# Kernel tuning notes

Measured on AMD Instinct MI355X. Metric: run time of the kernel, lower is better.

## Reference

```python
import jax, jax.numpy as jnp
import numpy as np
from jax import lax

K = 3
STRIDE = 1
PAD = 1
DIL = 1
EPS = 1e-5


def conv2d(x, w, b):
    y = lax.conv_general_dilated(
        x, w, (STRIDE, STRIDE), [(PAD, PAD), (PAD, PAD)],
        rhs_dilation=(DIL, DIL), dimension_numbers=('NCHW', 'OIHW', 'NCHW'))
    return y + b[None, :, None, None]


def deform_conv(x, offset, w):
    # x: [B,C,H,W], offset: [B,2*K2,Ho,Wo] (dy,dx interleaved per tap), w: [O,C,K,K]
    B, C, H, W = x.shape
    O = w.shape[0]
    K2 = K * K
    Ho, Wo = offset.shape[2], offset.shape[3]
    ky, kx = jnp.meshgrid(jnp.arange(K), jnp.arange(K), indexing='ij')
    # base sampling grid per kernel tap: [K2,Ho,Wo] (broadcast)
    by = (ky.reshape(K2, 1, 1) * DIL).astype(x.dtype) + (jnp.arange(Ho) * STRIDE - PAD).astype(x.dtype).reshape(1, Ho, 1)
    bx = (kx.reshape(K2, 1, 1) * DIL).astype(x.dtype) + (jnp.arange(Wo) * STRIDE - PAD).astype(x.dtype).reshape(1, 1, Wo)
    off = offset.reshape(B, K2, 2, Ho, Wo)
    py = by[None] + off[:, :, 0]  # [B,K2,Ho,Wo]
    px = bx[None] + off[:, :, 1]
    y0 = jnp.floor(py)
    x0 = jnp.floor(px)
    wy = py - y0
    wx = px - x0
    y0i = y0.astype(jnp.int32)
    x0i = x0.astype(jnp.int32)
    x_flat = x.reshape(B, C, H * W)

    def corner(yi, xi, cw):
        valid = ((yi >= 0) & (yi < H) & (xi >= 0) & (xi < W)).astype(x.dtype)
        idx = (jnp.clip(yi, 0, H - 1) * W + jnp.clip(xi, 0, W - 1)).reshape(B, -1)
        v = jax.vmap(lambda xb, ib: xb[:, ib])(x_flat, idx)  # [B,C,K2*Ho*Wo]
        return v * (cw * valid).reshape(B, 1, -1)

    val = (corner(y0i, x0i, (1 - wy) * (1 - wx))
           + corner(y0i, x0i + 1, (1 - wy) * wx)
           + corner(y0i + 1, x0i, wy * (1 - wx))
           + corner(y0i + 1, x0i + 1, wy * wx))  # [B,C,K2*Ho*Wo]
    samp = val.reshape(B, C, K2, Ho * Wo)
    out = jnp.einsum('bckp,ock->bop', samp, w.reshape(O, C, K2))
    return out.reshape(B, O, Ho, Wo)


def bn_gelu(x, gamma, beta):
    m = x.mean((0, 2, 3), keepdims=True)
    v = x.var((0, 2, 3), keepdims=True)
    xn = (x - m) / jnp.sqrt(v + EPS) * gamma[None, :, None, None] + beta[None, :, None, None]
    return jax.nn.gelu(xn, approximate=False)


def deform_block(x, w_off, b_off, w_def, gamma, beta):
    offset = conv2d(x, w_off, b_off)
    return bn_gelu(deform_conv(x, offset, w_def), gamma, beta)


def setup_inputs() -> dict:
    key = jax.random.key(0)
    ks = jax.random.split(key, 8)
    B, C, H, W = 4, 128, 112, 112
    fan = C * K * K
    x = jax.random.normal(ks[0], (B, C, H, W), jnp.float32)
    # offset conv weights: small random (original inits to 0; randomized to exercise sampling)
    w_off1 = jax.random.normal(ks[1], (2 * K * K, C, K, K), jnp.float32) * 0.01
    b_off1 = jnp.zeros((2 * K * K,), jnp.float32)
    w_def1 = jax.random.normal(ks[2], (C, C, K, K), jnp.float32) / np.sqrt(fan)
    gamma1 = jnp.ones((C,), jnp.float32)
    beta1 = jnp.zeros((C,), jnp.float32)
    w_off2 = jax.random.normal(ks[3], (2 * K * K, C, K, K), jnp.float32) * 0.01
    b_off2 = jnp.zeros((2 * K * K,), jnp.float32)
    w_def2 = jax.random.normal(ks[4], (C, C, K, K), jnp.float32) / np.sqrt(fan)
    gamma2 = jnp.ones((C,), jnp.float32)
    beta2 = jnp.zeros((C,), jnp.float32)
    return dict(x=x, w_off1=w_off1, b_off1=b_off1, w_def1=w_def1, gamma1=gamma1, beta1=beta1,
                w_off2=w_off2, b_off2=b_off2, w_def2=w_def2, gamma2=gamma2, beta2=beta2)


def reference(x, w_off1, b_off1, w_def1, gamma1, beta1,
              w_off2, b_off2, w_def2, gamma2, beta2):
    inp = x
    x = deform_block(x, w_off1, b_off1, w_def1, gamma1, beta1)
    x = deform_block(x, w_off2, b_off2, w_def2, gamma2, beta2)
    return x + inp
```

## Files before the change

### kernel.cpp

```cpp
#include <hip/hip_runtime.h>
#include <hip/hip_bf16.h>
#include <math.h>

#define HW 12544
#define CC 128
#define BB 4

typedef short bf16x8 __attribute__((ext_vector_type(8)));
typedef float f32x4 __attribute__((ext_vector_type(4)));

__device__ __forceinline__ float bf2f(unsigned int u) {
  union { unsigned int i; float f; } v; v.i = u << 16; return v.f;
}
__device__ __forceinline__ unsigned short f2bf(float f) {
  __hip_bfloat16 h = __float2bfloat16(f);
  return *reinterpret_cast<unsigned short*>(&h);
}
__device__ __forceinline__ float gelu(float v) {
  return 0.5f * v * (1.f + erff(v * 0.70710678118654752f));
}
__device__ __forceinline__ unsigned uc4(const uint4& v, int q) {
  return q == 0 ? v.x : q == 1 ? v.y : q == 2 ? v.z : v.w;
}

__global__ __launch_bounds__(256) void to_nhwc(const float* __restrict__ x,
                                               unsigned short* __restrict__ xh) {
  const int pt = blockIdx.x, ct = blockIdx.y, b = blockIdx.z;
  const int p0 = pt * 32, c0 = ct * 32;
  const int tid = threadIdx.x;
  __shared__ float ls[32][33];
  int col = tid & 31, r = tid >> 5;
#pragma unroll
  for (int i = 0; i < 4; i++) {
    int c = c0 + r + i * 8;
    ls[r + i * 8][col] = x[((size_t)(b * CC) + c) * HW + p0 + col];
  }
  __syncthreads();
  int px = tid >> 3, cq = (tid & 7) * 4;
  ushort4 v;
  v.x = f2bf(ls[cq + 0][px]);
  v.y = f2bf(ls[cq + 1][px]);
  v.z = f2bf(ls[cq + 2][px]);
  v.w = f2bf(ls[cq + 3][px]);
  *(ushort4*)&xh[((size_t)(b * HW) + p0 + px) * CC + c0 + cq] = v;
}

__global__ void pack_all(const float* __restrict__ wd1, const float* __restrict__ wo1,
                         const float* __restrict__ wd2, const float* __restrict__ wo2,
                         unsigned short* __restrict__ wpk1, unsigned short* __restrict__ wopk1,
                         unsigned short* __restrict__ wpk2, unsigned short* __restrict__ wopk2) {
  int i = blockIdx.x * 256 + threadIdx.x;
  if (i < 294912) {
    int ii = (i < 147456) ? i : i - 147456;
    const float* src = (i < 147456) ? wd1 : wd2;
    unsigned short* dst = (i < 147456) ? wpk1 : wpk2;
    int j = ii & 7, lane = (ii >> 3) & 63, ks = (ii >> 9) & 3, mo = (ii >> 11) & 7, k2 = ii >> 14;
    int o = mo * 16 + (lane & 15), c = ks * 32 + ((lane >> 4) << 3) + j;
    dst[ii] = f2bf(src[(o * CC + c) * 9 + k2]);
  } else {
    int ii = i - 294912;
    const float* src = (ii < 36864) ? wo1 : wo2;
    unsigned short* dst = (ii < 36864) ? wopk1 : wopk2;
    ii = (ii < 36864) ? ii : ii - 36864;
    int j = ii & 7, lane = (ii >> 3) & 63, ks = (ii >> 9) & 3, mo = (ii >> 11) & 1, k2 = ii >> 12;
    int o = mo * 16 + (lane & 15), c = ks * 32 + ((lane >> 4) << 3) + j;
    dst[ii] = (o < 18) ? f2bf(src[(o * CC + c) * 9 + k2]) : (unsigned short)0;
  }
}

__global__ __launch_bounds__(256) void offset_mfma(
    const unsigned short* __restrict__ xh, const unsigned short* __restrict__ wopk,
    const float* __restrict__ boff, float* __restrict__ offs2) {
  const int bid0 = blockIdx.x;
  const int bid = (bid0 & 7) * 196 + (bid0 >> 3);
  const int b = bid / 392;
  const int p0 = (bid % 392) * 32;
  const int tid = threadIdx.x;
  const int l = tid & 63, w = tid >> 6;
  const int hl = l & 15, ph = l >> 4;
  const int row = l & 15, grp = l >> 4;
  const int pxg = (w >> 1) * 16;
  const int mw = w & 1;
  __shared__ unsigned short s_smp[2][4096];
  const unsigned short* xb = xh + (size_t)b * HW * CC + hl * 8;
  f32x4 acc = (f32x4){0.f, 0.f, 0.f, 0.f};
  uint4 g2[2];
  bf16x8 af[4];

#define OISSUE(K2T)                                                            \
  {                                                                            \
    int ky = (K2T) / 3, kx = (K2T) % 3;                                        \
    _Pragma("unroll") for (int s = 0; s < 2; s++) {                            \
      int pxl = w * 8 + s * 4 + ph;                                            \
      int p = p0 + pxl;                                                        \
      int ho = p / 112, wo = p - ho * 112;                                     \
      int y = ho + ky - 1, x = wo + kx - 1;                                    \
      uint4 t = make_uint4(0u, 0u, 0u, 0u);                                    \
      if (((unsigned)y < 112u) & ((unsigned)x < 112u))                         \
        t = *(const uint4*)&xb[(size_t)(y * 112 + x) * CC];                    \
      g2[s] = t;                                                               \
    }                                                                          \
  }

#define OCOMMIT(BNBUF)                                                         \
  _Pragma("unroll") for (int s = 0; s < 2; s++) {                              \
    int pxl = w * 8 + s * 4 + ph;                                              \
    *(uint4*)((char*)&s_smp[BNBUF][0] +                                        \
              ((pxl * 256 + hl * 16) ^ ((pxl & 7) << 4))) = g2[s];             \
  }

#define OMFMA(BCBUF, ksB)                                                      \
  __builtin_amdgcn_s_setprio(1);                                               \
  _Pragma("unroll") for (int ks = ksB; ks < ksB + 2; ks++) {                   \
    int pxr = pxg + row;                                                       \
    bf16x8 bfr = *(const bf16x8*)((const char*)&s_smp[BCBUF][0] +              \
                 ((pxr * 256 + ks * 64 + grp * 16) ^ ((pxr & 7) << 4)));       \
    acc = __builtin_amdgcn_mfma_f32_16x16x32_bf16(af[ks], bfr, acc, 0, 0, 0);  \
  }                                                                            \
  __builtin_amdgcn_s_setprio(0);

#define OLOADW(K2T)                                                            \
  {                                                                            \
    const unsigned short* wb = wopk + (size_t)(K2T) * 4096;                    \
    _Pragma("unroll") for (int ks = 0; ks < 4; ks++)                           \
      af[ks] = *(const bf16x8*)&wb[(mw * 4 + ks) * 512 + l * 8];               \
  }

#define OITER(K2T, BC, BN)                                                     \
  {                                                                            \
    if ((K2T) < 8) { OISSUE((K2T) + 1); }                                      \
    OMFMA(BC, 0);                                                              \
    if ((K2T) < 8) { OCOMMIT(BN); }                                            \
    OMFMA(BC, 2);                                                              \
    if ((K2T) < 8) { OLOADW((K2T) + 1); __syncthreads(); }                     \
  }

  OISSUE(0); OCOMMIT(0); OLOADW(0);
  __syncthreads();
  OITER(0, 0, 1) OITER(1, 1, 0) OITER(2, 0, 1) OITER(3, 1, 0) OITER(4, 0, 1)
  OITER(5, 1, 0) OITER(6, 0, 1) OITER(7, 1, 0) OITER(8, 0, 1)
#undef OISSUE
#undef OCOMMIT
#undef OMFMA
#undef OLOADW
#undef OITER

  int p = p0 + pxg + row;
  if (mw == 0) {
    float2 w0 = make_float2(acc[0] + boff[grp * 4 + 0], acc[1] + boff[grp * 4 + 1]);
    float2 w1 = make_float2(acc[2] + boff[grp * 4 + 2], acc[3] + boff[grp * 4 + 3]);
    *(float2*)&offs2[((size_t)(b * 9 + grp * 2) * HW + p) * 2] = w0;
    *(float2*)&offs2[((size_t)(b * 9 + grp * 2 + 1) * HW + p) * 2] = w1;
  } else if (grp == 0) {
    float2 w2 = make_float2(acc[0] + boff[16], acc[1] + boff[17]);
    *(float2*)&offs2[((size_t)(b * 9 + 8) * HW + p) * 2] = w2;
  }
}

__global__ __launch_bounds__(256, 3) void deform_mfma(
    const unsigned short* __restrict__ xh, const float* __restrict__ offs2,
    const unsigned short* __restrict__ wpk, unsigned short* __restrict__ zh,
    float* __restrict__ part) {
  const int bid0 = blockIdx.x;
  const int bid = (bid0 & 7) * 196 + (bid0 >> 3);
  const int b = bid / 392;
  const int p0 = (bid % 392) * 32;
  const int tid = threadIdx.x;
  const int l = tid & 63, w = tid >> 6;
  const int hl = l & 15, ph = l >> 4;
  const int row = l & 15, grp = l >> 4;
  __shared__ unsigned short s_smp[2][4096];
  __shared__ uint4 s_coord[9][32];

  for (int e = tid; e < 288; e += 256) {
    int k2 = e >> 5, px = e & 31;
    int p = p0 + px;
    int ho = p / 112, wo = p - ho * 112;
    int ky = k2 / 3, kx = k2 - 3 * ky;
    float2 dv = *(const float2*)&offs2[((size_t)(b * 9 + k2) * HW + p) * 2];
    float py = (float)(ho + ky - 1) + dv.x;
    float pxf = (float)(wo + kx - 1) + dv.y;
    float y0f = floorf(py), x0f = floorf(pxf);
    float wy = py - y0f, wx = pxf - x0f;
    int y0 = (int)y0f, x0 = (int)x0f;
    int y1 = y0 + 1, x1 = x0 + 1;
    bool iy0 = ((unsigned)y0 < 112u), iy1 = ((unsigned)y1 < 112u);
    bool ix0 = ((unsigned)x0 < 112u), ix1 = ((unsigned)x1 < 112u);
    float v00 = (iy0 & ix0) ? (1.f - wy) * (1.f - wx) : 0.f;
    float v01 = (iy0 & ix1) ? (1.f - wy) * wx : 0.f;
    float v10 = (iy1 & ix0) ? wy * (1.f - wx) : 0.f;
    float v11 = (iy1 & ix1) ? wy * wx : 0.f;
    int y0c = min(max(y0, 0), 111), y1c = min(max(y1, 0), 111);
    int x0c = min(max(x0, 0), 111), x1c = min(max(x1, 0), 111);
    uint4 ce;
    ce.x = (unsigned)(y0c * 112 + x0c) | ((unsigned)(y0c * 112 + x1c) << 16);
    ce.y = (unsigned)(y1c * 112 + x0c) | ((unsigned)(y1c * 112 + x1c) << 16);
    ce.z = (unsigned)f2bf(v00) | ((unsigned)f2bf(v01) << 16);
    ce.w = (unsigned)f2bf(v10) | ((unsigned)f2bf(v11) << 16);
    s_coord[k2][px] = ce;
  }

  const unsigned short* xb = xh + (size_t)b * HW * CC + hl * 8;
  f32x4 acc[2][2];
#pragma unroll
  for (int m = 0; m < 2; m++)
#pragma unroll
    for (int n = 0; n < 2; n++) acc[m][n] = (f32x4){0.f, 0.f, 0.f, 0.f};
  uint4 g[2][4];
  uint2 wts[2];
  bf16x8 af[2][4];
  __syncthreads();

#define DISSUE(K2T)                                                            \
  _Pragma("unroll") for (int s = 0; s < 2; s++) {                              \
    int pxl = w * 8 + s * 4 + ph;                                              \
    uint4 cc = s_coord[K2T][pxl];                                              \
    wts[s] = make_uint2(cc.z, cc.w);                                           \
    g[s][0] = *(const uint4*)&xb[(size_t)(cc.x & 0xffffu) * CC];               \
    g[s][1] = *(const uint4*)&xb[(size_t)(cc.x >> 16) * CC];                   \
    g[s][2] = *(const uint4*)&xb[(size_t)(cc.y & 0xffffu) * CC];               \
    g[s][3] = *(const uint4*)&xb[(size_t)(cc.y >> 16) * CC];                   \
  }

#define DCOMMIT(BNBUF)                                                         \
  _Pragma("unroll") for (int s = 0; s < 2; s++) {                              \
    int pxl = w * 8 + s * 4 + ph;                                              \
    float w00 = bf2f(wts[s].x & 0xffffu), w01 = bf2f(wts[s].x >> 16);          \
    float w10 = bf2f(wts[s].y & 0xffffu), w11 = bf2f(wts[s].y >> 16);          \
    unsigned rr[4];                                                            \
    _Pragma("unroll") for (int q = 0; q < 4; q++) {                            \
      unsigned a0 = uc4(g[s][0], q), a1 = uc4(g[s][1], q);                     \
      unsigned a2 = uc4(g[s][2], q), a3 = uc4(g[s][3], q);                     \
      float elo = w00 * bf2f(a0 & 0xffffu) + w01 * bf2f(a1 & 0xffffu)          \
                + w10 * bf2f(a2 & 0xffffu) + w11 * bf2f(a3 & 0xffffu);         \
      float ehi = w00 * bf2f(a0 >> 16) + w01 * bf2f(a1 >> 16)                  \
                + w10 * bf2f(a2 >> 16) + w11 * bf2f(a3 >> 16);                 \
      rr[q] = (unsigned)f2bf(elo) | ((unsigned)f2bf(ehi) << 16);               \
    }                                                                          \
    *(uint4*)((char*)&s_smp[BNBUF][0] +                                        \
              ((pxl * 256 + hl * 16) ^ ((pxl & 7) << 4))) =                    \
        make_uint4(rr[0], rr[1], rr[2], rr[3]);                                \
  }

#define DMFMA(BCBUF, ksB)                                                      \
  __builtin_amdgcn_s_setprio(1);                                               \
  _Pragma("unroll") for (int ks = ksB; ks < ksB + 2; ks++) {                   \
    bf16x8 bfr[2];                                                             \
    _Pragma("unroll") for (int n = 0; n < 2; n++) {                            \
      int pxr = n * 16 + row;                                                  \
      bfr[n] = *(const bf16x8*)((const char*)&s_smp[BCBUF][0] +                \
               ((pxr * 256 + ks * 64 + grp * 16) ^ ((pxr & 7) << 4)));         \
    }                                                                          \
    _Pragma("unroll") for (int m = 0; m < 2; m++)                              \
      _Pragma("unroll") for (int n = 0; n < 2; n++)                            \
        acc[m][n] = __builtin_amdgcn_mfma_f32_16x16x32_bf16(af[m][ks], bfr[n], acc[m][n], 0, 0, 0); \
  }                                                                            \
  __builtin_amdgcn_s_setprio(0);

#define DLOADW(K2T)                                                            \
  {                                                                            \
    const unsigned short* wb = wpk + (size_t)((K2T) * 8 + w * 2) * 2048;       \
    _Pragma("unroll") for (int m = 0; m < 2; m++)                              \
      _Pragma("unroll") for (int ks = 0; ks < 4; ks++)                         \
        af[m][ks] = *(const bf16x8*)&wb[(m * 4 + ks) * 512 + l * 8];           \
  }

#define DITER(K2T, BC, BN)                                                     \
  {                                                                            \
    if ((K2T) < 8) { DISSUE((K2T) + 1); }                                      \
    DMFMA(BC, 0);                                                              \
    if ((K2T) < 8) { DCOMMIT(BN); }                                            \
    DMFMA(BC, 2);                                                              \
    if ((K2T) < 8) { DLOADW((K2T) + 1); __syncthreads(); }                     \
  }

  DISSUE(0); DCOMMIT(0); DLOADW(0);
  __syncthreads();
  DITER(0, 0, 1) DITER(1, 1, 0) DITER(2, 0, 1) DITER(3, 1, 0) DITER(4, 0, 1)
  DITER(5, 1, 0) DITER(6, 0, 1) DITER(7, 1, 0) DITER(8, 0, 1)
#undef DISSUE
#undef DCOMMIT
#undef DMFMA
#undef DLOADW
#undef DITER

#pragma unroll
  for (int m = 0; m < 2; m++)
#pragma unroll
    for (int n = 0; n < 2; n++) {
      int o = (w * 2 + m) * 16 + grp * 4;
      size_t px = (size_t)(b * HW) + p0 + n * 16 + row;
      unsigned lo = (unsigned)f2bf(acc[m][n][0]) | ((unsigned)f2bf(acc[m][n][1]) << 16);
      unsigned hi = (unsigned)f2bf(acc[m][n][2]) | ((unsigned)f2bf(acc[m][n][3]) << 16);
      *(uint2*)&zh[px * CC + o] = make_uint2(lo, hi);
    }

  float sv[8], qv[8];
#pragma unroll
  for (int m = 0; m < 2; m++)
#pragma unroll
    for (int r = 0; r < 4; r++) {
      float s = 0.f, q = 0.f;
#pragma unroll
      for (int n = 0; n < 2; n++) { float v = acc[m][n][r]; s += v; q += v * v; }
      sv[m * 4 + r] = s; qv[m * 4 + r] = q;
    }
#pragma unroll
  for (int d = 1; d < 16; d <<= 1)
#pragma unroll
    for (int i = 0; i < 8; i++) {
      sv[i] += __shfl_xor(sv[i], d);
      qv[i] += __shfl_xor(qv[i], d);
    }
  if (row == 0) {
#pragma unroll
    for (int m = 0; m < 2; m++)
#pragma unroll
      for (int r = 0; r < 4; r++) {
        int ch = (w * 2 + m) * 16 + grp * 4 + r;
        part[(size_t)ch * 1568 + bid] = sv[m * 4 + r];
        part[(size_t)(128 + ch) * 1568 + bid] = qv[m * 4 + r];
      }
  }
}

__global__ __launch_bounds__(256) void bn_fin(const float* __restrict__ part,
                                              const float* __restrict__ gamma,
                                              const float* __restrict__ beta,
                                              float* __restrict__ stats) {
  const int c = blockIdx.x, t = threadIdx.x;
  float s = 0.f, q = 0.f;
  for (int j = t; j < 1568; j += 256) {
    s += part[(size_t)c * 1568 + j];
    q += part[(size_t)(128 + c) * 1568 + j];
  }
  __shared__ float ss[256], sq2[256];
  ss[t] = s; sq2[t] = q;
  __syncthreads();
  for (int d = 128; d > 0; d >>= 1) {
    if (t < d) { ss[t] += ss[t + d]; sq2[t] += sq2[t + d]; }
    __syncthreads();
  }
  if (t == 0) {
    float N = 50176.f;
    float m = ss[0] / N;
    float var = sq2[0] / N - m * m;
    stats[c] = m;
    stats[128 + c] = rsqrtf(var + 1e-5f) * gamma[c];
    stats[256 + c] = beta[c];
  }
}

__global__ __launch_bounds__(256) void bn_gelu_to_bf16(
    const unsigned short* __restrict__ zh, const float* __restrict__ stats,
    unsigned short* __restrict__ yh) {
  int i = blockIdx.x * 256 + threadIdx.x;
  int c0 = (i & 15) * 8;
  uint4 zv = ((const uint4*)zh)[i];
  f32x4 m0 = *(const f32x4*)&stats[c0], m1 = *(const f32x4*)&stats[c0 + 4];
  f32x4 r0 = *(const f32x4*)&stats[128 + c0], r1 = *(const f32x4*)&stats[128 + c0 + 4];
  f32x4 b0 = *(const f32x4*)&stats[256 + c0], b1 = *(const f32x4*)&stats[256 + c0 + 4];
  float v[8] = {bf2f(zv.x & 0xffffu), bf2f(zv.x >> 16), bf2f(zv.y & 0xffffu), bf2f(zv.y >> 16),
                bf2f(zv.z & 0xffffu), bf2f(zv.z >> 16), bf2f(zv.w & 0xffffu), bf2f(zv.w >> 16)};
  unsigned o[4];
#pragma unroll
  for (int j = 0; j < 4; j++) {
    float mj0 = (j < 2) ? m0[j * 2] : m1[j * 2 - 4], mj1 = (j < 2) ? m0[j * 2 + 1] : m1[j * 2 - 3];
    float rj0 = (j < 2) ? r0[j * 2] : r1[j * 2 - 4], rj1 = (j < 2) ? r0[j * 2 + 1] : r1[j * 2 - 3];
    float bj0 = (j < 2) ? b0[j * 2] : b1[j * 2 - 4], bj1 = (j < 2) ? b0[j * 2 + 1] : b1[j * 2 - 3];
    float e0 = gelu((v[j * 2] - mj0) * rj0 + bj0);
    float e1 = gelu((v[j * 2 + 1] - mj1) * rj1 + bj1);
    o[j] = (unsigned)f2bf(e0) | ((unsigned)f2bf(e1) << 16);
  }
  ((uint4*)yh)[i] = make_uint4(o[0], o[1], o[2], o[3]);
}

__global__ __launch_bounds__(256) void bn_gelu_final(
    const unsigned short* __restrict__ zh, const float* __restrict__ stats,
    const float* __restrict__ x, float* __restrict__ out) {
  const int pt = blockIdx.x, b = blockIdx.y;
  const int p0 = pt * 16;
  const int tid = threadIdx.x;
  __shared__ float ls[16][129];
  {
    int cq = tid & 15, r = tid >> 4;
    uint4 zv = *(const uint4*)&zh[((size_t)(b * HW) + p0 + r) * CC + cq * 8];
    float v[8] = {bf2f(zv.x & 0xffffu), bf2f(zv.x >> 16), bf2f(zv.y & 0xffffu), bf2f(zv.y >> 16),
                  bf2f(zv.z & 0xffffu), bf2f(zv.z >> 16), bf2f(zv.w & 0xffffu), bf2f(zv.w >> 16)};
    f32x4 m0 = *(const f32x4*)&stats[cq * 8], m1 = *(const f32x4*)&stats[cq * 8 + 4];
    f32x4 r0 = *(const f32x4*)&stats[128 + cq * 8], r1 = *(const f32x4*)&stats[128 + cq * 8 + 4];
    f32x4 b0 = *(const f32x4*)&stats[256 + cq * 8], b1 = *(const f32x4*)&stats[256 + cq * 8 + 4];
#pragma unroll
    for (int j = 0; j < 4; j++) {
      ls[r][cq * 8 + j] = gelu((v[j] - m0[j]) * r0[j] + b0[j]);
      ls[r][cq * 8 + 4 + j] = gelu((v[4 + j] - m1[j]) * r1[j] + b1[j]);
    }
  }
  __syncthreads();
  int c = tid & 127, half = tid >> 7;
  const float* xr = x + ((size_t)(b * CC) + c) * HW + p0 + half * 8;
  float* orow = out + ((size_t)(b * CC) + c) * HW + p0 + half * 8;
  float4 o1 = make_float4(ls[half * 8 + 0][c], ls[half * 8 + 1][c],
                          ls[half * 8 + 2][c], ls[half * 8 + 3][c]);
  float4 o2 = make_float4(ls[half * 8 + 4][c], ls[half * 8 + 5][c],
                          ls[half * 8 + 6][c], ls[half * 8 + 7][c]);
  float4 x1 = *(const float4*)&xr[0];
  float4 x2 = *(const float4*)&xr[4];
  o1.x += x1.x; o1.y += x1.y; o1.z += x1.z; o1.w += x1.w;
  o2.x += x2.x; o2.y += x2.y; o2.z += x2.z; o2.w += x2.w;
  *(float4*)&orow[0] = o1;
  *(float4*)&orow[4] = o2;
}

extern "C" void kernel_launch(void* const* d_in, const int* in_sizes, int n_in,
                              void* d_out, int out_size, void* d_ws, size_t ws_size,
                              hipStream_t stream) {
  const float* x = (const float*)d_in[0];
  const float* w_off1 = (const float*)d_in[1];
  const float* b_off1 = (const float*)d_in[2];
  const float* w_def1 = (const float*)d_in[3];
  const float* gamma1 = (const float*)d_in[4];
  const float* beta1 = (const float*)d_in[5];
  const float* w_off2 = (const float*)d_in[6];
  const float* b_off2 = (const float*)d_in[7];
  const float* w_def2 = (const float*)d_in[8];
  const float* gamma2 = (const float*)d_in[9];
  const float* beta2 = (const float*)d_in[10];
  float* out = (float*)d_out;

  char* ws = (char*)d_ws;
  unsigned short* xhb = (unsigned short*)ws;
  unsigned short* zhb = (unsigned short*)(ws + 12845056);
  float* offb = (float*)(ws + 25690112);
  unsigned short* wpk1 = (unsigned short*)(ws + 29302784);
  unsigned short* wpk2 = (unsigned short*)(ws + 29597696);
  unsigned short* wopk1 = (unsigned short*)(ws + 29892608);
  unsigned short* wopk2 = (unsigned short*)(ws + 29966336);
  float* partb = (float*)(ws + 30040064);
  float* statsb = (float*)(ws + 31645696);

  to_nhwc<<<dim3(392, 4, 4), 256, 0, stream>>>(x, xhb);
  pack_all<<<1440, 256, 0, stream>>>(w_def1, w_off1, w_def2, w_off2,
                                     wpk1, wopk1, wpk2, wopk2);

  offset_mfma<<<1568, 256, 0, stream>>>(xhb, wopk1, b_off1, offb);
  deform_mfma<<<1568, 256, 0, stream>>>(xhb, offb, wpk1, zhb, partb);
  bn_fin<<<128, 256, 0, stream>>>(partb, gamma1, beta1, statsb);
  bn_gelu_to_bf16<<<3136, 256, 0, stream>>>(zhb, statsb, xhb);

  offset_mfma<<<1568, 256, 0, stream>>>(xhb, wopk2, b_off2, offb);
  deform_mfma<<<1568, 256, 0, stream>>>(xhb, offb, wpk2, zhb, partb);
  bn_fin<<<128, 256, 0, stream>>>(partb, gamma2, beta2, statsb);
  bn_gelu_final<<<dim3(784, 4), 256, 0, stream>>>(zhb, statsb, x, out);
}
```

Baseline: 172.5 us.

## Halve deform conv pixel tile to 16 per block, doubling grid size

Shrinks the per-block pixel tile in the deformable conv kernel from 32 to 16 pixels, so each wave gathers one pixel group per tap instead of two and issues half as many MFMAs per weight fragment. The grid doubles to 3136 blocks, which adds parallelism and cuts per-thread registers and LDS, which may help occupancy. In exchange, each weight fragment load is reused over fewer pixels, and the BN partial-sum buffer and its reduction double in size. The stats buffer offset moves to make room for the larger partials.

```diff
diff --git a/kernel.cpp b/kernel.cpp
--- a/kernel.cpp
+++ b/kernel.cpp
@@ -162,18 +162,18 @@
     const unsigned short* __restrict__ wpk, unsigned short* __restrict__ zh,
     float* __restrict__ part) {
   const int bid0 = blockIdx.x;
-  const int bid = (bid0 & 7) * 196 + (bid0 >> 3);
-  const int b = bid / 392;
-  const int p0 = (bid % 392) * 32;
+  const int bid = (bid0 & 7) * 392 + (bid0 >> 3);
+  const int b = bid / 784;
+  const int p0 = (bid % 784) * 16;
   const int tid = threadIdx.x;
   const int l = tid & 63, w = tid >> 6;
   const int hl = l & 15, ph = l >> 4;
   const int row = l & 15, grp = l >> 4;
-  __shared__ unsigned short s_smp[2][4096];
-  __shared__ uint4 s_coord[9][32];
-
-  for (int e = tid; e < 288; e += 256) {
-    int k2 = e >> 5, px = e & 31;
+  __shared__ unsigned short s_smp[2][2048];
+  __shared__ uint4 s_coord[9][16];
+
+  for (int e = tid; e < 144; e += 256) {
+    int k2 = e >> 4, px = e & 15;
     int p = p0 + px;
     int ho = p / 112, wo = p - ho * 112;
     int ky = k2 / 3, kx = k2 - 3 * ky;
@@ -201,36 +201,34 @@
   }
 
   const unsigned short* xb = xh + (size_t)b * HW * CC + hl * 8;
-  f32x4 acc[2][2];
-#pragma unroll
-  for (int m = 0; m < 2; m++)
-#pragma unroll
-    for (int n = 0; n < 2; n++) acc[m][n] = (f32x4){0.f, 0.f, 0.f, 0.f};
-  uint4 g[2][4];
-  uint2 wts[2];
+  f32x4 acc[2];
+  acc[0] = (f32x4){0.f, 0.f, 0.f, 0.f};
+  acc[1] = (f32x4){0.f, 0.f, 0.f, 0.f};
+  uint4 g[4];
+  uint2 wts;
   bf16x8 af[2][4];
   __syncthreads();
 
 #define DISSUE(K2T)                                                            \
-  _Pragma("unroll") for (int s = 0; s < 2; s++) {                              \
-    int pxl = w * 8 + s * 4 + ph;                                              \
+  {                                                                            \
+    int pxl = w * 4 + ph;                                                      \
     uint4 cc = s_coord[K2T][pxl];                                              \
-    wts[s] = make_uint2(cc.z, cc.w);                                           \
-    g[s][0] = *(const uint4*)&xb[(size_t)(cc.x & 0xffffu) * CC];               \
-    g[s][1] = *(const uint4*)&xb[(size_t)(cc.x >> 16) * CC];                   \
-    g[s][2] = *(const uint4*)&xb[(size_t)(cc.y & 0xffffu) * CC];               \
-    g[s][3] = *(const uint4*)&xb[(size_t)(cc.y >> 16) * CC];                   \
+    wts = make_uint2(cc.z, cc.w);                                              \
+    g[0] = *(const uint4*)&xb[(size_t)(cc.x & 0xffffu) * CC];                  \
+    g[1] = *(const uint4*)&xb[(size_t)(cc.x >> 16) * CC];                      \
+    g[2] = *(const uint4*)&xb[(size_t)(cc.y & 0xffffu) * CC];                  \
+    g[3] = *(const uint4*)&xb[(size_t)(cc.y >> 16) * CC];                      \
   }
 
 #define DCOMMIT(BNBUF)                                                         \
-  _Pragma("unroll") for (int s = 0; s < 2; s++) {                              \
-    int pxl = w * 8 + s * 4 + ph;                                              \
-    float w00 = bf2f(wts[s].x & 0xffffu), w01 = bf2f(wts[s].x >> 16);          \
-    float w10 = bf2f(wts[s].y & 0xffffu), w11 = bf2f(wts[s].y >> 16);          \
+  {                                                                            \
+    int pxl = w * 4 + ph;                                                      \
+    float w00 = bf2f(wts.x & 0xffffu), w01 = bf2f(wts.x >> 16);                \
+    float w10 = bf2f(wts.y & 0xffffu), w11 = bf2f(wts.y >> 16);                \
     unsigned rr[4];                                                            \
     _Pragma("unroll") for (int q = 0; q < 4; q++) {                            \
-      unsigned a0 = uc4(g[s][0], q), a1 = uc4(g[s][1], q);                     \
-      unsigned a2 = uc4(g[s][2], q), a3 = uc4(g[s][3], q);                     \
+      unsigned a0 = uc4(g[0], q), a1 = uc4(g[1], q);                           \
+      unsigned a2 = uc4(g[2], q), a3 = uc4(g[3], q);                           \
       float elo = w00 * bf2f(a0 & 0xffffu) + w01 * bf2f(a1 & 0xffffu)          \
                 + w10 * bf2f(a2 & 0xffffu) + w11 * bf2f(a3 & 0xffffu);         \
       float ehi = w00 * bf2f(a0 >> 16) + w01 * bf2f(a1 >> 16)                  \
@@ -245,15 +243,10 @@
 #define DMFMA(BCBUF, ksB)                                                      \
   __builtin_amdgcn_s_setprio(1);                                               \
   _Pragma("unroll") for (int ks = ksB; ks < ksB + 2; ks++) {                   \
-    bf16x8 bfr[2];                                                             \
-    _Pragma("unroll") for (int n = 0; n < 2; n++) {                            \
-      int pxr = n * 16 + row;                                                  \
-      bfr[n] = *(const bf16x8*)((const char*)&s_smp[BCBUF][0] +                \
-               ((pxr * 256 + ks * 64 + grp * 16) ^ ((pxr & 7) << 4)));         \
-    }                                                                          \
+    bf16x8 bfr = *(const bf16x8*)((const char*)&s_smp[BCBUF][0] +              \
+               ((row * 256 + ks * 64 + grp * 16) ^ ((row & 7) << 4)));         \
     _Pragma("unroll") for (int m = 0; m < 2; m++)                              \
-      _Pragma("unroll") for (int n = 0; n < 2; n++)                            \
-        acc[m][n] = __builtin_amdgcn_mfma_f32_16x16x32_bf16(af[m][ks], bfr[n], acc[m][n], 0, 0, 0); \
+      acc[m] = __builtin_amdgcn_mfma_f32_16x16x32_bf16(af[m][ks], bfr, acc[m], 0, 0, 0); \
   }                                                                            \
   __builtin_amdgcn_s_setprio(0);
 
@@ -285,25 +278,22 @@
 #undef DITER
 
 #pragma unroll
+  for (int m = 0; m < 2; m++) {
+    int o = (w * 2 + m) * 16 + grp * 4;
+    size_t px = (size_t)(b * HW) + p0 + row;
+    unsigned lo = (unsigned)f2bf(acc[m][0]) | ((unsigned)f2bf(acc[m][1]) << 16);
+    unsigned hi = (unsigned)f2bf(acc[m][2]) | ((unsigned)f2bf(acc[m][3]) << 16);
+    *(uint2*)&zh[px * CC + o] = make_uint2(lo, hi);
+  }
+
+  float sv[8], qv[8];
+#pragma unroll
   for (int m = 0; m < 2; m++)
 #pragma unroll
-    for (int n = 0; n < 2; n++) {
-      int o = (w * 2 + m) * 16 + grp * 4;
-      size_t px = (size_t)(b * HW) + p0 + n * 16 + row;
-      unsigned lo = (unsigned)f2bf(acc[m][n][0]) | ((unsigned)f2bf(acc[m][n][1]) << 16);
-      unsigned hi = (unsigned)f2bf(acc[m][n][2]) | ((unsigned)f2bf(acc[m][n][3]) << 16);
-      *(uint2*)&zh[px * CC + o] = make_uint2(lo, hi);
-    }
-
-  float sv[8], qv[8];
-#pragma unroll
-  for (int m = 0; m < 2; m++)
-#pragma unroll
     for (int r = 0; r < 4; r++) {
-      float s = 0.f, q = 0.f;
-#pragma unroll
-      for (int n = 0; n < 2; n++) { float v = acc[m][n][r]; s += v; q += v * v; }
-      sv[m * 4 + r] = s; qv[m * 4 + r] = q;
+      float v = acc[m][r];
+      sv[m * 4 + r] = v;
+      qv[m * 4 + r] = v * v;
     }
 #pragma unroll
   for (int d = 1; d < 16; d <<= 1)
@@ -318,8 +308,8 @@
 #pragma unroll
       for (int r = 0; r < 4; r++) {
         int ch = (w * 2 + m) * 16 + grp * 4 + r;
-        part[(size_t)ch * 1568 + bid] = sv[m * 4 + r];
-        part[(size_t)(128 + ch) * 1568 + bid] = qv[m * 4 + r];
+        part[(size_t)ch * 3136 + bid] = sv[m * 4 + r];
+        part[(size_t)(128 + ch) * 3136 + bid] = qv[m * 4 + r];
       }
   }
 }
@@ -330,9 +320,9 @@
                                               float* __restrict__ stats) {
   const int c = blockIdx.x, t = threadIdx.x;
   float s = 0.f, q = 0.f;
-  for (int j = t; j < 1568; j += 256) {
-    s += part[(size_t)c * 1568 + j];
-    q += part[(size_t)(128 + c) * 1568 + j];
+  for (int j = t; j < 3136; j += 256) {
+    s += part[(size_t)c * 3136 + j];
+    q += part[(size_t)(128 + c) * 3136 + j];
   }
   __shared__ float ss[256], sq2[256];
   ss[t] = s; sq2[t] = q;
@@ -437,19 +427,19 @@
   unsigned short* wopk1 = (unsigned short*)(ws + 29892608);
   unsigned short* wopk2 = (unsigned short*)(ws + 29966336);
   float* partb = (float*)(ws + 30040064);
-  float* statsb = (float*)(ws + 31645696);
+  float* statsb = (float*)(ws + 33251328);
 
   to_nhwc<<<dim3(392, 4, 4), 256, 0, stream>>>(x, xhb);
   pack_all<<<1440, 256, 0, stream>>>(w_def1, w_off1, w_def2, w_off2,
                                      wpk1, wopk1, wpk2, wopk2);
 
   offset_mfma<<<1568, 256, 0, stream>>>(xhb, wopk1, b_off1, offb);
-  deform_mfma<<<1568, 256, 0, stream>>>(xhb, offb, wpk1, zhb, partb);
+  deform_mfma<<<3136, 256, 0, stream>>>(xhb, offb, wpk1, zhb, partb);
   bn_fin<<<128, 256, 0, stream>>>(partb, gamma1, beta1, statsb);
   bn_gelu_to_bf16<<<3136, 256, 0, stream>>>(zhb, statsb, xhb);
 
   offset_mfma<<<1568, 256, 0, stream>>>(xhb, wopk2, b_off2, offb);
-  deform_mfma<<<1568, 256, 0, stream>>>(xhb, offb, wpk2, zhb, partb);
+  deform_mfma<<<3136, 256, 0, stream>>>(xhb, offb, wpk2, zhb, partb);
   bn_fin<<<128, 256, 0, stream>>>(partb, gamma2, beta2, statsb);
   bn_gelu_final<<<dim3(784, 4), 256, 0, stream>>>(zhb, statsb, x, out);
 }
```

Measured after the change: 194.8 us. +12.9%, slower.
